# Performance work log

Hardware: AMD Instinct MI355X
Metric: run time of the kernel (lower is better)

## Reference

```python
import jax, jax.numpy as jnp
import numpy as np

H, HD, D = 16, 64, 1024
SCALE = HD ** -0.5
TEMP = 1.0
EPS = 1e-5

def setup_inputs() -> dict:
    key = jax.random.key(0)
    ks = jax.random.split(key, 10)
    B, N = 2, 2048
    lim = 1.0 / np.sqrt(D)
    def lin(k, out_d, in_d):
        k1, k2 = jax.random.split(k)
        W = jax.random.uniform(k1, (out_d, in_d), jnp.float32, -lim, lim)
        b = jax.random.uniform(k2, (out_d,), jnp.float32, -lim, lim)
        return W, b
    Wq, bq = lin(ks[0], H * HD, D)
    Wk, bk = lin(ks[1], H * HD, D)
    Wv, bv = lin(ks[2], H * HD, D)
    Wo, bo = lin(ks[3], D, H * HD)
    return {
        "x": jax.random.normal(ks[4], (B, N, D), jnp.float32),
        "adaptive_scale": jnp.ones((H,), jnp.float32),
        "Wq": Wq, "bq": bq, "Wk": Wk, "bk": bk, "Wv": Wv, "bv": bv,
        "Wo": Wo, "bo": bo,
        "gamma": jnp.ones((D,), jnp.float32),
        "beta": jnp.zeros((D,), jnp.float32),
    }

def reference(x, adaptive_scale, Wq, bq, Wk, bk, Wv, bv, Wo, bo, gamma, beta):
    B, N, _ = x.shape
    # self-attention: context = x
    Q = (x @ Wq.T + bq).reshape(B, N, H, HD)
    K = (x @ Wk.T + bk).reshape(B, N, H, HD)
    V = (x @ Wv.T + bv).reshape(B, N, H, HD)
    # per-head adaptive scale folded into scores (matches naive QK^T * scale / temp)
    scores = jnp.einsum('bnhd,bmhd->bhnm', Q, K)
    scores = scores * (SCALE * adaptive_scale)[None, :, None, None] / TEMP
    w = jax.nn.softmax(scores, axis=-1)  # [B,H,N,N]
    attn = jnp.einsum('bhnm,bmhd->bnhd', w, V).reshape(B, N, H * HD)
    y = x + (attn @ Wo.T + bo)
    mu = jnp.mean(y, axis=-1, keepdims=True)
    var = jnp.var(y, axis=-1, keepdims=True)
    return (y - mu) / jnp.sqrt(var + EPS) * gamma + beta
```

## Files before the change

kernel.cpp:

```cpp
#include <hip/hip_runtime.h>
#include <hip/hip_bf16.h>

using bf16 = __hip_bfloat16;
typedef __attribute__((ext_vector_type(8))) short short8;
typedef __attribute__((ext_vector_type(4))) short short4v;
typedef __attribute__((ext_vector_type(4))) float f32x4;

#define MFMA16(a, b, c) __builtin_amdgcn_mfma_f32_16x16x32_bf16((a), (b), (c), 0, 0, 0)

__device__ inline void async16(bf16* lds, const bf16* g) {
  __builtin_amdgcn_global_load_lds(
      (const __attribute__((address_space(1))) void*)g,
      (__attribute__((address_space(3))) void*)lds, 16, 0, 0);
}

__device__ inline short bfs(float x) {
  union { bf16 h; short s; } u; u.h = __float2bfloat16(x); return u.s;
}
__device__ inline short4v pack4(float a, float b, float c, float d) {
  short4v r; r[0] = bfs(a); r[1] = bfs(b); r[2] = bfs(c); r[3] = bfs(d); return r;
}
__device__ inline short4v pack4t(float a, float b, float c, float d) {
  unsigned lo = __builtin_amdgcn_perm(__float_as_uint(b), __float_as_uint(a), 0x07060302u);
  unsigned hi = __builtin_amdgcn_perm(__float_as_uint(d), __float_as_uint(c), 0x07060302u);
  union { unsigned u[2]; short4v v; } r;
  r.u[0] = lo; r.u[1] = hi;
  return r.v;
}
__device__ inline float ex2(float x) {
  float r; asm("v_exp_f32 %0, %1" : "=v"(r) : "v"(x)); return r;
}

__global__ __launch_bounds__(256) void cvt_all(
    const float* __restrict__ x,  const float* __restrict__ Wq,
    const float* __restrict__ Wk, const float* __restrict__ Wv,
    const float* __restrict__ Wo,
    bf16* __restrict__ xb, bf16* __restrict__ Wqb, bf16* __restrict__ Wkb,
    bf16* __restrict__ Wvb, bf16* __restrict__ Wob) {
  int i = blockIdx.x * 256 + threadIdx.x;
  const float* s; bf16* d; int off;
  if (i < 1048576)      { s = x;  d = xb;  off = i; }
  else if (i < 1310720) { s = Wq; d = Wqb; off = i - 1048576; }
  else if (i < 1572864) { s = Wk; d = Wkb; off = i - 1310720; }
  else if (i < 1835008) { s = Wv; d = Wvb; off = i - 1572864; }
  else                  { s = Wo; d = Wob; off = i - 1835008; }
  float4 v = ((const float4*)s)[off];
  short4v o = pack4(v.x, v.y, v.z, v.w);
  *(short4v*)&d[(size_t)off * 4] = o;
}

__global__ __launch_bounds__(256) void gemm_qkv(
    const bf16* __restrict__ A,
    const bf16* __restrict__ Wq, const bf16* __restrict__ Wk, const bf16* __restrict__ Wv,
    const float* __restrict__ bq, const float* __restrict__ bk, const float* __restrict__ bv,
    const float* __restrict__ asc,
    bf16* __restrict__ Qb, bf16* __restrict__ Kb, bf16* __restrict__ Vtb) {
  __shared__ __align__(16) bf16 As[128 * 64];
  __shared__ __align__(16) bf16 Bs[128 * 64];
  __shared__ __align__(16) bf16 scrT[4][16 * 72];

  const int tid = threadIdx.x;
  const int lane = tid & 63;
  const int w = tid >> 6;
  const int m0 = blockIdx.x * 128;
  const int region = blockIdx.y >> 3;
  const int n0loc = (blockIdx.y & 7) * 128;
  const int wm = (w >> 1) * 64;
  const int wn = (w & 1) * 64;
  const int rq = lane & 15;
  const int quad = lane >> 4;

  const bf16* W = region == 0 ? Wq : (region == 1 ? Wk : Wv);
  const float* bias = region == 0 ? bq : (region == 1 ? bk : bv);
  bf16* C = region == 0 ? Qb : (region == 1 ? Kb : Vtb);

  f32x4 acc[4][4] = {};
  const bf16* Ag = A + (size_t)m0 * 1024;
  const bf16* Wg = W + (size_t)n0loc * 1024;

  const int srow = lane >> 3;
  const int sws = ((lane & 7) ^ srow) * 8;
  const int c0 = (quad ^ (rq & 7)) * 8;

  for (int k0 = 0; k0 < 1024; k0 += 64) {
    __syncthreads();
#pragma unroll
    for (int t = 0; t < 4; ++t) {
      int rb = w * 32 + t * 8;
      int row = rb + srow;
      async16(&As[rb * 64 + lane * 8], Ag + (size_t)row * 1024 + k0 + sws);
      async16(&Bs[rb * 64 + lane * 8], Wg + (size_t)row * 1024 + k0 + sws);
    }
    __syncthreads();

#pragma unroll
    for (int ks = 0; ks < 2; ++ks) {
      int off = c0 ^ (ks * 32);
      short8 a[4], b[4];
#pragma unroll
      for (int i = 0; i < 4; ++i) a[i] = *(const short8*)&As[(wm + i * 16 + rq) * 64 + off];
#pragma unroll
      for (int j = 0; j < 4; ++j) b[j] = *(const short8*)&Bs[(wn + j * 16 + rq) * 64 + off];
#pragma unroll
      for (int i = 0; i < 4; ++i)
#pragma unroll
        for (int j = 0; j < 4; ++j) acc[i][j] = MFMA16(a[i], b[j], acc[i][j]);
    }
  }

  const float LOG2E = 1.44269504088896f;
  if (region < 2) {
#pragma unroll
    for (int i = 0; i < 4; ++i)
#pragma unroll
      for (int j = 0; j < 4; ++j)
#pragma unroll
        for (int r2 = 0; r2 < 4; ++r2) {
          int m = m0 + wm + i * 16 + quad * 4 + r2;
          int nr = n0loc + wn + j * 16 + rq;
          int bb = m >> 11, t = m & 2047, h = nr >> 6, hd = nr & 63;
          float v = acc[i][j][r2] + bias[nr];
          if (region == 0) v *= 0.125f * asc[h] * LOG2E;
          C[(((size_t)(bb * 16 + h)) * 2048 + t) * 64 + hd] = __float2bfloat16(v);
        }
  } else {
    const int bb = m0 >> 11;
    const int h = (n0loc + wn) >> 6;
    const int tbase = (m0 & 2047) + wm;
    bf16* scr = scrT[w];
#pragma unroll
    for (int j = 0; j < 4; ++j) {
      int nr = n0loc + wn + j * 16 + rq;
      float bi = bias[nr];
#pragma unroll
      for (int i = 0; i < 4; ++i) {
        short4v pv = pack4(acc[i][j][0] + bi, acc[i][j][1] + bi,
                           acc[i][j][2] + bi, acc[i][j][3] + bi);
        *(short4v*)&scr[rq * 72 + i * 16 + quad * 4] = pv;
      }
#pragma unroll
      for (int pp = 0; pp < 4; ++pp) {
        int hdl = pp * 4 + quad;
        short4v v4 = *(const short4v*)&scr[hdl * 72 + rq * 4];
        size_t addr = (((size_t)(bb * 16 + h)) * 64 + j * 16 + hdl) * 2048 + tbase + rq * 4;
        *(short4v*)&C[addr] = v4;
      }
    }
  }
}

__global__ __launch_bounds__(256) void gemm_out(
    const bf16* __restrict__ A, const bf16* __restrict__ W,
    const float* __restrict__ bias, const float* __restrict__ R,
    float* __restrict__ Y) {
  __shared__ __align__(16) bf16 As[64 * 64];
  __shared__ __align__(16) bf16 Bs[128 * 64];

  const int tid = threadIdx.x;
  const int lane = tid & 63;
  const int w = tid >> 6;
  const int m0 = blockIdx.x * 64;
  const int n0 = blockIdx.y * 128;
  const int wm = (w >> 1) * 32;
  const int wn = (w & 1) * 64;
  const int rq = lane & 15;
  const int quad = lane >> 4;

  f32x4 acc[2][4] = {};
  const bf16* Ag = A + (size_t)m0 * 1024;
  const bf16* Wg = W + (size_t)n0 * 1024;

  const int srow = lane >> 3;
  const int sws = ((lane & 7) ^ srow) * 8;
  const int c0 = (quad ^ (rq & 7)) * 8;

  for (int k0 = 0; k0 < 1024; k0 += 64) {
    __syncthreads();
#pragma unroll
    for (int t = 0; t < 2; ++t) {
      int rb = w * 16 + t * 8;
      int row = rb + srow;
      async16(&As[rb * 64 + lane * 8], Ag + (size_t)row * 1024 + k0 + sws);
    }
#pragma unroll
    for (int t = 0; t < 4; ++t) {
      int rb = w * 32 + t * 8;
      int row = rb + srow;
      async16(&Bs[rb * 64 + lane * 8], Wg + (size_t)row * 1024 + k0 + sws);
    }
    __syncthreads();

#pragma unroll
    for (int ks = 0; ks < 2; ++ks) {
      int off = c0 ^ (ks * 32);
      short8 a[2], b[4];
#pragma unroll
      for (int i = 0; i < 2; ++i) a[i] = *(const short8*)&As[(wm + i * 16 + rq) * 64 + off];
#pragma unroll
      for (int j = 0; j < 4; ++j) b[j] = *(const short8*)&Bs[(wn + j * 16 + rq) * 64 + off];
#pragma unroll
      for (int i = 0; i < 2; ++i)
#pragma unroll
        for (int j = 0; j < 4; ++j) acc[i][j] = MFMA16(a[i], b[j], acc[i][j]);
    }
  }

#pragma unroll
  for (int i = 0; i < 2; ++i)
#pragma unroll
    for (int j = 0; j < 4; ++j)
#pragma unroll
      for (int r2 = 0; r2 < 4; ++r2) {
        int m = m0 + wm + i * 16 + quad * 4 + r2;
        int n = n0 + wn + j * 16 + rq;
        Y[(size_t)m * 1024 + n] = acc[i][j][r2] + bias[n] + R[(size_t)m * 1024 + n];
      }
}

#define LP 72
__global__ __launch_bounds__(256, 4) void attn_kernel(
    const bf16* __restrict__ Qb, const bf16* __restrict__ Kb,
    const bf16* __restrict__ Vtb,
    bf16* __restrict__ P0, bf16* __restrict__ P1, float* __restrict__ lbuf) {
  __shared__ __align__(16) bf16 Ks[64 * 64];
  __shared__ __align__(16) bf16 Vs[64 * 64];
  __shared__ __align__(16) bf16 Ps[4][32 * LP];

  const int wid = blockIdx.x + (blockIdx.y << 4) + (blockIdx.z << 8);
  const int sid = (wid & 7) * 128 + (wid >> 3);
  const int q0 = (sid & 15) * 128;
  const int h = (sid >> 4) & 15;
  const int zz = sid >> 8;
  const int b = zz & 1;
  const int half = zz >> 1;

  const int tid = threadIdx.x;
  const int lane = tid & 63;
  const int w = tid >> 6;
  const int rq = lane & 15;
  const int quad = lane >> 4;
  const int kq = quad * 8;

  const size_t head = ((size_t)(b * 16 + h)) * 2048 * 64;
  const bf16* Qh = Qb + head;
  const bf16* Kh = Kb + head;
  const bf16* Vh = Vtb + head;

  short8 aq[2][2];
#pragma unroll
  for (int s = 0; s < 2; ++s) {
    const bf16* qrow = Qh + (size_t)(q0 + w * 32 + s * 16 + rq) * 64;
    aq[s][0] = *(const short8*)&qrow[kq];
    aq[s][1] = *(const short8*)&qrow[kq + 32];
  }

  short8 ones;
#pragma unroll
  for (int i = 0; i < 8; ++i) ones[i] = (short)0x3F80;

  const int srow = lane >> 3;
  const int swsV = ((lane & 7) ^ srow) * 8;
  const int c0 = (quad ^ (rq & 7)) * 8;
  const int c1 = c0 ^ 32;

  f32x4 accO[2][4] = {};
  f32x4 lacc[2] = {};

  const int kt0 = half * 16;
  for (int kt = kt0; kt < kt0 + 16; ++kt) {
    __syncthreads();
#pragma unroll
    for (int t = 0; t < 2; ++t) {
      int rb = w * 16 + t * 8;
      int row = rb + srow;
      int swsK = ((lane & 7) ^ ((row >> 2) & 7)) * 8;
      async16(&Ks[rb * 64 + lane * 8], Kh + (size_t)(kt * 64 + row) * 64 + swsK);
      async16(&Vs[rb * 64 + lane * 8], Vh + (size_t)row * 2048 + kt * 64 + swsV);
    }
    __syncthreads();

    short8 bk[4][2];
#pragma unroll
    for (int j = 0; j < 4; ++j) {
      const bf16* kr = &Ks[(rq * 4 + j) * 64];
      bk[j][0] = *(const short8*)&kr[c0];
      bk[j][1] = *(const short8*)&kr[c1];
    }

#pragma unroll
    for (int s = 0; s < 2; ++s) {
      f32x4 S[4] = {};
      __builtin_amdgcn_s_setprio(1);
#pragma unroll
      for (int j = 0; j < 4; ++j) {
        S[j] = MFMA16(aq[s][0], bk[j][0], S[j]);
        S[j] = MFMA16(aq[s][1], bk[j][1], S[j]);
      }
      __builtin_amdgcn_s_setprio(0);
#pragma unroll
      for (int r = 0; r < 4; ++r) {
        short4v pv = pack4t(ex2(S[0][r]), ex2(S[1][r]),
                            ex2(S[2][r]), ex2(S[3][r]));
        *(short4v*)&Ps[w][(s * 16 + quad * 4 + r) * LP + rq * 4] = pv;
      }
    }

    short8 bv[4][2];
#pragma unroll
    for (int dt = 0; dt < 4; ++dt) {
      const bf16* vr = &Vs[(dt * 16 + rq) * 64];
      bv[dt][0] = *(const short8*)&vr[c0];
      bv[dt][1] = *(const short8*)&vr[c1];
    }
#pragma unroll
    for (int s = 0; s < 2; ++s) {
      short8 ap0 = *(const short8*)&Ps[w][(s * 16 + rq) * LP + kq];
      short8 ap1 = *(const short8*)&Ps[w][(s * 16 + rq) * LP + kq + 32];
      __builtin_amdgcn_s_setprio(1);
#pragma unroll
      for (int dt = 0; dt < 4; ++dt) {
        accO[s][dt] = MFMA16(ap0, bv[dt][0], accO[s][dt]);
        accO[s][dt] = MFMA16(ap1, bv[dt][1], accO[s][dt]);
      }
      lacc[s] = MFMA16(ap0, ones, lacc[s]);
      lacc[s] = MFMA16(ap1, ones, lacc[s]);
      __builtin_amdgcn_s_setprio(0);
    }
  }

  bf16* Pout = half ? P1 : P0;
  float* lout = lbuf + half * 65536;
#pragma unroll
  for (int s = 0; s < 2; ++s) {
#pragma unroll
    for (int dt = 0; dt < 4; ++dt)
#pragma unroll
      for (int r = 0; r < 4; ++r) {
        int t = q0 + w * 32 + s * 16 + quad * 4 + r;
        int d = dt * 16 + rq;
        Pout[((size_t)(b * 2048 + t)) * 1024 + h * 64 + d] =
            __float2bfloat16(accO[s][dt][r]);
      }
    if (rq == 0) {
#pragma unroll
      for (int r = 0; r < 4; ++r) {
        int t = q0 + w * 32 + s * 16 + quad * 4 + r;
        lout[(b * 16 + h) * 2048 + t] = lacc[s][r];
      }
    }
  }
}

__global__ __launch_bounds__(256) void combine_kernel(
    bf16* __restrict__ P0, const bf16* __restrict__ P1,
    const float* __restrict__ lbuf) {
  const int row = blockIdx.x;
  const int tid = threadIdx.x;
  const int col = tid * 4;
  const int b = row >> 11, t = row & 2047;
  const int h = col >> 6;
  const float l = lbuf[(b * 16 + h) * 2048 + t] + lbuf[65536 + (b * 16 + h) * 2048 + t];
  const float rl = 1.f / l;
  size_t base = (size_t)row * 1024 + col;
  short4v p0 = *(const short4v*)&P0[base];
  short4v p1 = *(const short4v*)&P1[base];
  union { short s; bf16 h; } u;
  float v[4];
#pragma unroll
  for (int i = 0; i < 4; ++i) {
    u.s = p0[i]; float a = __bfloat162float(u.h);
    u.s = p1[i]; float c = __bfloat162float(u.h);
    v[i] = (a + c) * rl;
  }
  *(short4v*)&P0[base] = pack4(v[0], v[1], v[2], v[3]);
}

__global__ __launch_bounds__(256) void ln_kernel(
    const float* __restrict__ Y, const float* __restrict__ gamma,
    const float* __restrict__ beta, float* __restrict__ out) {
  const int row = blockIdx.x;
  const int tid = threadIdx.x;
  const int lane = tid & 63;
  const int w = tid >> 6;
  const float* y = Y + (size_t)row * 1024;

  float4 v = *(const float4*)&y[tid * 4];
  float s = v.x + v.y + v.z + v.w;
  float ss = v.x * v.x + v.y * v.y + v.z * v.z + v.w * v.w;
#pragma unroll
  for (int msk = 1; msk < 64; msk <<= 1) {
    s += __shfl_xor(s, msk);
    ss += __shfl_xor(ss, msk);
  }
  __shared__ float red[2][4];
  if (lane == 0) { red[0][w] = s; red[1][w] = ss; }
  __syncthreads();
  s = red[0][0] + red[0][1] + red[0][2] + red[0][3];
  ss = red[1][0] + red[1][1] + red[1][2] + red[1][3];
  float mean = s * (1.f / 1024.f);
  float var = ss * (1.f / 1024.f) - mean * mean;
  float rstd = rsqrtf(var + 1e-5f);
  float4 g = *(const float4*)&gamma[tid * 4];
  float4 bt = *(const float4*)&beta[tid * 4];
  float4 o;
  o.x = (v.x - mean) * rstd * g.x + bt.x;
  o.y = (v.y - mean) * rstd * g.y + bt.y;
  o.z = (v.z - mean) * rstd * g.z + bt.z;
  o.w = (v.w - mean) * rstd * g.w + bt.w;
  *(float4*)&out[(size_t)row * 1024 + tid * 4] = o;
}

extern "C" void kernel_launch(void* const* d_in, const int* in_sizes, int n_in,
                              void* d_out, int out_size, void* d_ws, size_t ws_size,
                              hipStream_t stream) {
  const float* x     = (const float*)d_in[0];
  const float* asc   = (const float*)d_in[1];
  const float* Wq    = (const float*)d_in[2];
  const float* bq    = (const float*)d_in[3];
  const float* Wk    = (const float*)d_in[4];
  const float* bk    = (const float*)d_in[5];
  const float* Wv    = (const float*)d_in[6];
  const float* bv    = (const float*)d_in[7];
  const float* Wo    = (const float*)d_in[8];
  const float* bo    = (const float*)d_in[9];
  const float* gamma = (const float*)d_in[10];
  const float* beta  = (const float*)d_in[11];
  float* out = (float*)d_out;

  char* ws = (char*)d_ws;
  const size_t MB = 1024 * 1024;
  bf16* Qb   = (bf16*)(ws);
  bf16* Kb   = (bf16*)(ws + 8 * MB);
  bf16* Vtb  = (bf16*)(ws + 16 * MB);
  bf16* attn = (bf16*)(ws + 24 * MB);
  bf16* xb   = (bf16*)(ws + 32 * MB);
  bf16* Wqb  = (bf16*)(ws + 40 * MB);
  bf16* Wkb  = (bf16*)(ws + 42 * MB);
  bf16* Wvb  = (bf16*)(ws + 44 * MB);
  bf16* Wob  = (bf16*)(ws + 46 * MB);
  float* y   = (float*)(ws);
  bf16* P1   = xb;
  float* lbuf = (float*)Wqb;

  cvt_all<<<dim3(8192), dim3(256), 0, stream>>>(x, Wq, Wk, Wv, Wo, xb, Wqb, Wkb, Wvb, Wob);
  gemm_qkv<<<dim3(32, 24), dim3(256), 0, stream>>>(xb, Wqb, Wkb, Wvb, bq, bk, bv, asc, Qb, Kb, Vtb);
  attn_kernel<<<dim3(16, 16, 4), dim3(256), 0, stream>>>(Qb, Kb, Vtb, attn, P1, lbuf);
  combine_kernel<<<dim3(4096), dim3(256), 0, stream>>>(attn, P1, lbuf);
  gemm_out<<<dim3(64, 8), dim3(256), 0, stream>>>(attn, Wob, bo, x, y);
  ln_kernel<<<dim3(4096), dim3(256), 0, stream>>>(y, gamma, beta, out);
}
```

Measured before the change: 210.6 us.

## Keep attention P tile in registers via permlane swaps instead of LDS

The attention kernel now computes S transposed (K as the A operand, Q as B) so that each lane holds exponentiated scores along the key dimension. It then uses v_permlane32_swap and v_permlane16_swap to rearrange them into the A-operand layout for the PV MFMA, which removes the per-wave Ps LDS buffer along with its stores and reloads. The K LDS swizzle and read offsets change to match the new access pattern. This cuts LDS traffic and shared memory per block, at the cost of more cross-lane permute instructions and a layout mapping that is easy to get wrong.

```diff
diff --git a/kernel.cpp b/kernel.cpp
--- a/kernel.cpp
+++ b/kernel.cpp
@@ -20,15 +20,17 @@
 __device__ inline short4v pack4(float a, float b, float c, float d) {
   short4v r; r[0] = bfs(a); r[1] = bfs(b); r[2] = bfs(c); r[3] = bfs(d); return r;
 }
-__device__ inline short4v pack4t(float a, float b, float c, float d) {
-  unsigned lo = __builtin_amdgcn_perm(__float_as_uint(b), __float_as_uint(a), 0x07060302u);
-  unsigned hi = __builtin_amdgcn_perm(__float_as_uint(d), __float_as_uint(c), 0x07060302u);
-  union { unsigned u[2]; short4v v; } r;
-  r.u[0] = lo; r.u[1] = hi;
-  return r.v;
+__device__ inline unsigned pkt2(float x, float y) {
+  return __builtin_amdgcn_perm(__float_as_uint(y), __float_as_uint(x), 0x07060302u);
 }
 __device__ inline float ex2(float x) {
   float r; asm("v_exp_f32 %0, %1" : "=v"(r) : "v"(x)); return r;
+}
+__device__ inline void pl32swap(unsigned& a, unsigned& b) {
+  asm("v_permlane32_swap_b32 %0, %1" : "+v"(a), "+v"(b));
+}
+__device__ inline void pl16swap(unsigned& a, unsigned& b) {
+  asm("v_permlane16_swap_b32 %0, %1" : "+v"(a), "+v"(b));
 }
 
 __global__ __launch_bounds__(256) void cvt_all(
@@ -217,14 +219,12 @@
       }
 }
 
-#define LP 72
 __global__ __launch_bounds__(256, 4) void attn_kernel(
     const bf16* __restrict__ Qb, const bf16* __restrict__ Kb,
     const bf16* __restrict__ Vtb,
     bf16* __restrict__ P0, bf16* __restrict__ P1, float* __restrict__ lbuf) {
   __shared__ __align__(16) bf16 Ks[64 * 64];
   __shared__ __align__(16) bf16 Vs[64 * 64];
-  __shared__ __align__(16) bf16 Ps[4][32 * LP];
 
   const int wid = blockIdx.x + (blockIdx.y << 4) + (blockIdx.z << 8);
   const int sid = (wid & 7) * 128 + (wid >> 3);
@@ -239,7 +239,6 @@
   const int w = tid >> 6;
   const int rq = lane & 15;
   const int quad = lane >> 4;
-  const int kq = quad * 8;
 
   const size_t head = ((size_t)(b * 16 + h)) * 2048 * 64;
   const bf16* Qh = Qb + head;
@@ -250,8 +249,8 @@
 #pragma unroll
   for (int s = 0; s < 2; ++s) {
     const bf16* qrow = Qh + (size_t)(q0 + w * 32 + s * 16 + rq) * 64;
-    aq[s][0] = *(const short8*)&qrow[kq];
-    aq[s][1] = *(const short8*)&qrow[kq + 32];
+    aq[s][0] = *(const short8*)&qrow[quad * 8];
+    aq[s][1] = *(const short8*)&qrow[quad * 8 + 32];
   }
 
   short8 ones;
@@ -262,6 +261,8 @@
   const int swsV = ((lane & 7) ^ srow) * 8;
   const int c0 = (quad ^ (rq & 7)) * 8;
   const int c1 = c0 ^ 32;
+  const int kc0 = (quad ^ (rq >> 1)) * 8;
+  const int kc1 = kc0 ^ 32;
 
   f32x4 accO[2][4] = {};
   f32x4 lacc[2] = {};
@@ -273,59 +274,65 @@
     for (int t = 0; t < 2; ++t) {
       int rb = w * 16 + t * 8;
       int row = rb + srow;
-      int swsK = ((lane & 7) ^ ((row >> 2) & 7)) * 8;
+      int swsK = ((lane & 7) ^ ((row >> 1) & 7)) * 8;
       async16(&Ks[rb * 64 + lane * 8], Kh + (size_t)(kt * 64 + row) * 64 + swsK);
       async16(&Vs[rb * 64 + lane * 8], Vh + (size_t)row * 2048 + kt * 64 + swsV);
     }
     __syncthreads();
 
-    short8 bk[4][2];
-#pragma unroll
-    for (int j = 0; j < 4; ++j) {
-      const bf16* kr = &Ks[(rq * 4 + j) * 64];
-      bk[j][0] = *(const short8*)&kr[c0];
-      bk[j][1] = *(const short8*)&kr[c1];
-    }
-
+    f32x4 S[2][4] = {};
+    __builtin_amdgcn_s_setprio(1);
+#pragma unroll
+    for (int c = 0; c < 4; ++c) {
+      const bf16* kr = &Ks[(c * 16 + rq) * 64];
+      short8 k0 = *(const short8*)&kr[kc0];
+      short8 k1 = *(const short8*)&kr[kc1];
+      S[0][c] = MFMA16(k0, aq[0][0], S[0][c]);
+      S[0][c] = MFMA16(k1, aq[0][1], S[0][c]);
+      S[1][c] = MFMA16(k0, aq[1][0], S[1][c]);
+      S[1][c] = MFMA16(k1, aq[1][1], S[1][c]);
+    }
+    __builtin_amdgcn_s_setprio(0);
+
+    unsigned W[2][8];
+#pragma unroll
+    for (int s = 0; s < 2; ++s)
+#pragma unroll
+      for (int c = 0; c < 4; ++c) {
+        W[s][c * 2 + 0] = pkt2(ex2(S[s][c][0]), ex2(S[s][c][1]));
+        W[s][c * 2 + 1] = pkt2(ex2(S[s][c][2]), ex2(S[s][c][3]));
+      }
+
+    short8 ap[2][2];
 #pragma unroll
     for (int s = 0; s < 2; ++s) {
-      f32x4 S[4] = {};
-      __builtin_amdgcn_s_setprio(1);
-#pragma unroll
-      for (int j = 0; j < 4; ++j) {
-        S[j] = MFMA16(aq[s][0], bk[j][0], S[j]);
-        S[j] = MFMA16(aq[s][1], bk[j][1], S[j]);
-      }
-      __builtin_amdgcn_s_setprio(0);
-#pragma unroll
-      for (int r = 0; r < 4; ++r) {
-        short4v pv = pack4t(ex2(S[0][r]), ex2(S[1][r]),
-                            ex2(S[2][r]), ex2(S[3][r]));
-        *(short4v*)&Ps[w][(s * 16 + quad * 4 + r) * LP + rq * 4] = pv;
-      }
-    }
-
-    short8 bv[4][2];
+      pl32swap(W[s][0], W[s][2]); pl32swap(W[s][1], W[s][3]);
+      pl32swap(W[s][4], W[s][6]); pl32swap(W[s][5], W[s][7]);
+      pl16swap(W[s][0], W[s][2]); pl16swap(W[s][1], W[s][3]);
+      pl16swap(W[s][4], W[s][6]); pl16swap(W[s][5], W[s][7]);
+      union { unsigned u[4]; short8 v; } f0, f1;
+      f0.u[0] = W[s][0]; f0.u[1] = W[s][1]; f0.u[2] = W[s][2]; f0.u[3] = W[s][3];
+      f1.u[0] = W[s][4]; f1.u[1] = W[s][5]; f1.u[2] = W[s][6]; f1.u[3] = W[s][7];
+      ap[s][0] = f0.v; ap[s][1] = f1.v;
+    }
+
+    __builtin_amdgcn_s_setprio(1);
 #pragma unroll
     for (int dt = 0; dt < 4; ++dt) {
       const bf16* vr = &Vs[(dt * 16 + rq) * 64];
-      bv[dt][0] = *(const short8*)&vr[c0];
-      bv[dt][1] = *(const short8*)&vr[c1];
+      short8 v0 = *(const short8*)&vr[c0];
+      short8 v1 = *(const short8*)&vr[c1];
+      accO[0][dt] = MFMA16(ap[0][0], v0, accO[0][dt]);
+      accO[0][dt] = MFMA16(ap[0][1], v1, accO[0][dt]);
+      accO[1][dt] = MFMA16(ap[1][0], v0, accO[1][dt]);
+      accO[1][dt] = MFMA16(ap[1][1], v1, accO[1][dt]);
     }
 #pragma unroll
     for (int s = 0; s < 2; ++s) {
-      short8 ap0 = *(const short8*)&Ps[w][(s * 16 + rq) * LP + kq];
-      short8 ap1 = *(const short8*)&Ps[w][(s * 16 + rq) * LP + kq + 32];
-      __builtin_amdgcn_s_setprio(1);
-#pragma unroll
-      for (int dt = 0; dt < 4; ++dt) {
-        accO[s][dt] = MFMA16(ap0, bv[dt][0], accO[s][dt]);
-        accO[s][dt] = MFMA16(ap1, bv[dt][1], accO[s][dt]);
-      }
-      lacc[s] = MFMA16(ap0, ones, lacc[s]);
-      lacc[s] = MFMA16(ap1, ones, lacc[s]);
-      __builtin_amdgcn_s_setprio(0);
-    }
+      lacc[s] = MFMA16(ap[s][0], ones, lacc[s]);
+      lacc[s] = MFMA16(ap[s][1], ones, lacc[s]);
+    }
+    __builtin_amdgcn_s_setprio(0);
   }
 
   bf16* Pout = half ? P1 : P0;
```

Measured after the change: 206.5 us, median of 2. About the same (-1.9%).
